# Performance work log

Hardware: AMD Instinct MI355X
Metric: run time of the kernel (lower is better)

The kernel has to match this reference:

```python
import jax, jax.numpy as jnp
import numpy as np

H = 256          # hidden_dim
D = 64           # dim_dynamic
R = 49           # pooler_resolution ** 2
N = 2000         # bs * num_proposals
EPS = 1e-5


def _ln(x, g, b):
    m = jnp.mean(x, axis=-1, keepdims=True)
    v = jnp.mean(jnp.square(x - m), axis=-1, keepdims=True)
    return (x - m) * jax.lax.rsqrt(v + EPS) * g + b


def setup_inputs() -> dict:
    key = jax.random.key(0)
    ks = jax.random.split(key, 6)
    pro_features = jax.random.normal(ks[0], (1, N, H), dtype=jnp.float32)
    roi_features = jax.random.normal(ks[1], (R, N, H), dtype=jnp.float32)
    # dynamic_layer: Linear(H, num_dynamic * H * D) with num_dynamic = 2
    W_dyn = jax.random.normal(ks[2], (H, 2 * H * D), dtype=jnp.float32) * 0.02
    b_dyn = jnp.zeros((2 * H * D,), dtype=jnp.float32)
    # out_layer: Linear(H * R, H)
    W_out = jax.random.normal(ks[3], (H * R, H), dtype=jnp.float32) * 0.02
    b_out = jnp.zeros((H,), dtype=jnp.float32)
    g1 = jnp.ones((D,), dtype=jnp.float32); b1 = jnp.zeros((D,), dtype=jnp.float32)
    g2 = jnp.ones((H,), dtype=jnp.float32); b2 = jnp.zeros((H,), dtype=jnp.float32)
    g3 = jnp.ones((H,), dtype=jnp.float32); b3 = jnp.zeros((H,), dtype=jnp.float32)
    return {"pro_features": pro_features, "roi_features": roi_features,
            "W_dyn": W_dyn, "b_dyn": b_dyn, "W_out": W_out, "b_out": b_out,
            "g1": g1, "b1": b1, "g2": g2, "b2": b2, "g3": g3, "b3": b3}


def reference(pro_features, roi_features, W_dyn, b_dyn, W_out, b_out,
              g1, b1, g2, b2, g3, b3):
    # roi_features: (R, N, H) -> features: (N, R, H)
    feats = jnp.transpose(roi_features, (1, 0, 2))
    # per-instance dynamic parameters: (N, 2*H*D)
    params = pro_features[0] @ W_dyn + b_dyn
    num_params = H * D
    p1 = params[:, :num_params].reshape(-1, H, D)   # (N, H, D)
    p2 = params[:, num_params:].reshape(-1, D, H)   # (N, D, H)
    f = jnp.einsum('nrh,nhd->nrd', feats, p1)       # bmm 1
    f = jax.nn.relu(_ln(f, g1, b1))
    f = jnp.einsum('nrd,ndh->nrh', f, p2)           # bmm 2
    f = jax.nn.relu(_ln(f, g2, b2))
    f = f.reshape(f.shape[0], R * H)                # flatten(1)
    f = jax.nn.relu(_ln(f @ W_out + b_out, g3, b3))
    return f  # (N, H)
```

## Files before the change

### kernel.cpp

```cpp
#include <hip/hip_runtime.h>

typedef unsigned short u16;
typedef __attribute__((ext_vector_type(8))) short short8;
typedef __attribute__((ext_vector_type(4))) float f32x4;

#define N_INST 2000
#define H_DIM 256
#define D_DIM 64
#define R_DIM 49
#define LN_EPS 1e-5f
#define SPLITK 14

__device__ __forceinline__ u16 f2bf(float f) {
  union { float f; unsigned int i; } x; x.f = f;
  unsigned int r = x.i + 0x7fffu + ((x.i >> 16) & 1u);
  return (u16)(r >> 16);
}
__device__ __forceinline__ float bf2f(u16 u) {
  union { unsigned int i; float f; } x; x.i = ((unsigned int)u) << 16; return x.f;
}
__device__ __forceinline__ short8 ld8(const u16* p) {
  return *reinterpret_cast<const short8*>(p);
}
__device__ __forceinline__ short8 pack8(float4 a, float4 b) {
  short8 r;
  r[0] = (short)f2bf(a.x); r[1] = (short)f2bf(a.y);
  r[2] = (short)f2bf(a.z); r[3] = (short)f2bf(a.w);
  r[4] = (short)f2bf(b.x); r[5] = (short)f2bf(b.y);
  r[6] = (short)f2bf(b.z); r[7] = (short)f2bf(b.w);
  return r;
}
__device__ __forceinline__ f32x4 mfma16(short8 a, short8 b, f32x4 c) {
  return __builtin_amdgcn_mfma_f32_16x16x32_bf16(a, b, c, 0, 0, 0);
}
__device__ __forceinline__ void gload16(const u16* g, u16* l) {
  __builtin_amdgcn_global_load_lds(
      (const __attribute__((address_space(1))) void*)g,
      (__attribute__((address_space(3))) void*)l, 16, 0, 0);
}

__global__ __launch_bounds__(256) void prep_all(
    const float* __restrict__ pro,  u16* __restrict__ proB,
    const float* __restrict__ Wdyn, u16* __restrict__ WdynT,
    const float* __restrict__ Wout, u16* __restrict__ WoutT) {
  __shared__ u16 T[64][65];
  const int tid = threadIdx.x;
  const int wave = tid >> 6, lane = tid & 63;
  const int b = blockIdx.x;
  if (b < 2048) {
    const int half = b >> 10;
    const int bb = b & 1023;
    const int kt = bb >> 8;
    long colbase, rowbase; int rstride;
    if (half == 0) {
      int h = bb & 255;
      colbase = (long)h * 64; rowbase = h; rstride = 256;
    } else {
      int d = bb & 63, hc = (bb >> 6) & 3;
      colbase = 16384L + d * 256 + hc * 64;
      rowbase = 16384L + hc * 4096 + d; rstride = 64;
    }
#pragma unroll
    for (int i = 0; i < 16; ++i) {
      int kk = wave * 16 + i;
      int k = kt * 64 + kk;
      T[kk][lane] = f2bf(Wdyn[(long)k * 32768 + colbase + lane]);
    }
    __syncthreads();
#pragma unroll
    for (int i = 0; i < 16; ++i) {
      int jj = wave * 16 + i;
      long ro = rowbase + (long)jj * rstride;
      WdynT[ro * 256 + kt * 64 + lane] = T[lane][jj];
    }
  } else if (b < 2832) {
    const int b2 = b - 2048;
    const int kt = b2 >> 2, ct = b2 & 3;
#pragma unroll
    for (int i = 0; i < 16; ++i) {
      int kk = wave * 16 + i;
      long k = (long)kt * 64 + kk;
      T[kk][lane] = f2bf(Wout[k * 256 + ct * 64 + lane]);
    }
    __syncthreads();
#pragma unroll
    for (int i = 0; i < 16; ++i) {
      int cc = wave * 16 + i;
      long c = (long)ct * 64 + cc;
      WoutT[c * 12544 + (long)kt * 64 + lane] = T[lane][cc];
    }
  } else {
    const int n4 = 128000;
    for (int i = (b - 2832) * 256 + tid; i < n4; i += 500 * 256) {
      float4 v = ((const float4*)pro)[i];
      u16* op = proB + i * 4;
      op[0] = f2bf(v.x); op[1] = f2bf(v.y); op[2] = f2bf(v.z); op[3] = f2bf(v.w);
    }
  }
}

__global__ __launch_bounds__(256, 3) void gemm128(
    const u16* __restrict__ A, int lda, int M,
    const u16* __restrict__ BT, int ldbt,
    const float* __restrict__ bias, int bias_mode,
    void* __restrict__ Cout, int ldc, long c_stride_s,
    int ksteps, int n_blocks, int out_f32)
{
  union Smem {
    struct { u16 a[2][128 * 32]; u16 b[2][128 * 32]; } s;
    u16 cb[128 * 128];
  };
  __shared__ Smem sm;

  const int tid = threadIdx.x;
  const int wave = tid >> 6, lane = tid & 63;
  const int quad = lane >> 4, l16 = lane & 15;
  const int wm = wave >> 1, wn = wave & 1;
  const int bid = blockIdx.x;
  const int mblk = bid / n_blocks, nblk = bid - mblk * n_blocks;
  const int m0 = mblk * 128, n0 = nblk * 128;
  const int s = blockIdx.y;
  const int kb = s * ksteps * 32;

  const int cl = tid & 3;
  const int r0 = tid >> 2, r1 = 64 + (tid >> 2);
  const int cg0 = cl ^ ((r0 >> 1) & 3);
  const int cg1 = cl ^ ((r1 >> 1) & 3);
  int ga0 = m0 + r0; if (ga0 >= M) ga0 = M - 1;
  int ga1 = m0 + r1; if (ga1 >= M) ga1 = M - 1;
  const u16* gA0 = A + (long)ga0 * lda + kb + cg0 * 8;
  const u16* gA1 = A + (long)ga1 * lda + kb + cg1 * 8;
  const u16* gB0 = BT + (long)(n0 + r0) * ldbt + kb + cg0 * 8;
  const u16* gB1 = BT + (long)(n0 + r1) * ldbt + kb + cg1 * 8;

  int fAoff[4], fBoff[4];
#pragma unroll
  for (int i = 0; i < 4; ++i) {
    int rt = wm * 64 + i * 16 + l16;
    fAoff[i] = rt * 32 + (quad ^ ((rt >> 1) & 3)) * 8;
    int ct = wn * 64 + i * 16 + l16;
    fBoff[i] = ct * 32 + (quad ^ ((ct >> 1) & 3)) * 8;
  }

  f32x4 acc[4][4];
#pragma unroll
  for (int mi = 0; mi < 4; ++mi)
#pragma unroll
    for (int ni = 0; ni < 4; ++ni) acc[mi][ni] = f32x4{0.f, 0.f, 0.f, 0.f};

  gload16(gA0, &sm.s.a[0][tid * 8]);
  gload16(gA1, &sm.s.a[0][(tid + 256) * 8]);
  gload16(gB0, &sm.s.b[0][tid * 8]);
  gload16(gB1, &sm.s.b[0][(tid + 256) * 8]);

  for (int ks = 0; ks < ksteps; ++ks) {
    const int cur = ks & 1, nxt = cur ^ 1;
    __syncthreads();
    if (ks + 1 < ksteps) {
      const int ko = (ks + 1) * 32;
      gload16(gA0 + ko, &sm.s.a[nxt][tid * 8]);
      gload16(gA1 + ko, &sm.s.a[nxt][(tid + 256) * 8]);
      gload16(gB0 + ko, &sm.s.b[nxt][tid * 8]);
      gload16(gB1 + ko, &sm.s.b[nxt][(tid + 256) * 8]);
    }
    short8 av[4], bv[4];
#pragma unroll
    for (int i = 0; i < 4; ++i) {
      av[i] = ld8(&sm.s.a[cur][fAoff[i]]);
      bv[i] = ld8(&sm.s.b[cur][fBoff[i]]);
    }
#pragma unroll
    for (int mi = 0; mi < 4; ++mi)
#pragma unroll
      for (int ni = 0; ni < 4; ++ni)
        acc[mi][ni] = mfma16(av[mi], bv[ni], acc[mi][ni]);
  }

  if (!out_f32) {
    float bvv[4];
#pragma unroll
    for (int ni = 0; ni < 4; ++ni) {
      int col = n0 + wn * 64 + ni * 16 + l16;
      int bi = col;
      if (bias_mode == 3)
        bi = (col < 16384) ? (((col & 255) << 6) + (col >> 8))
                           : (16384 + ((col & 63) << 8) + ((col >> 6) & 255));
      bvv[ni] = bias ? bias[bi] : 0.f;
    }
    __syncthreads();
#pragma unroll
    for (int mi = 0; mi < 4; ++mi)
#pragma unroll
      for (int ni = 0; ni < 4; ++ni)
#pragma unroll
        for (int i = 0; i < 4; ++i) {
          int row = wm * 64 + mi * 16 + quad * 4 + i;
          int col = wn * 64 + ni * 16 + l16;
          sm.cb[row * 128 + col] = f2bf(acc[mi][ni][i] + bvv[ni]);
        }
    __syncthreads();
    u16* Cp = (u16*)Cout;
#pragma unroll
    for (int j = 0; j < 8; ++j) {
      int lin = j * 2048 + tid * 8;
      int row = lin >> 7, col = lin & 127;
      int grow = m0 + row;
      if (grow < M)
        *reinterpret_cast<short8*>(Cp + (long)grow * ldc + n0 + col) =
            ld8(&sm.cb[lin]);
    }
  } else {
    float* Cp = (float*)Cout + (long)s * c_stride_s;
#pragma unroll
    for (int mi = 0; mi < 4; ++mi)
#pragma unroll
      for (int ni = 0; ni < 4; ++ni) {
        int col = n0 + wn * 64 + ni * 16 + l16;
#pragma unroll
        for (int i = 0; i < 4; ++i) {
          int row = m0 + wm * 64 + mi * 16 + quad * 4 + i;
          if (row < M) Cp[(long)row * ldc + col] = acc[mi][ni][i];
        }
      }
  }
}

__global__ __launch_bounds__(256, 4) void bmm12_ln(
    const float* __restrict__ roi,
    const u16* __restrict__ P12,
    const float* __restrict__ g1, const float* __restrict__ b1,
    const float* __restrict__ g2, const float* __restrict__ b2,
    u16* __restrict__ f2n)
{
  __shared__ __align__(16) u16 p1b[16384];
  __shared__ __align__(16) u16 f1b[4096];
  const int n = blockIdx.x;
  const int tid = threadIdx.x;
  const int wave = tid >> 6, lane = tid & 63;
  const int quad = lane >> 4, l16 = lane & 15;
  const int wstripe = wave * 16;

  const u16* P1n = P12 + (long)n * 32768;
#pragma unroll
  for (int j = 0; j < 8; ++j) {
    int lc = j * 256 + tid;
    int d = lc >> 5, c = lc & 31;
    int cg = (c & 24) | ((c & 7) ^ (d & 7));
    gload16(P1n + d * 256 + cg * 8, &p1b[lc * 8]);
  }
  int r = wstripe + l16;
  int rr = (r < R_DIM) ? r : 0;
  const float* Arow = roi + ((long)rr * N_INST + n) * H_DIM + quad * 8;
  short8 sa[8];
#pragma unroll
  for (int ks = 0; ks < 8; ++ks) {
    float4 va = ((const float4*)(Arow + ks * 32))[0];
    float4 vb = ((const float4*)(Arow + ks * 32))[1];
    sa[ks] = pack8(va, vb);
  }
  const u16* P2n = P12 + (long)n * 32768 + 16384;
  short8 pf[4][2];
#pragma unroll
  for (int hs = 0; hs < 4; ++hs)
#pragma unroll
    for (int ks = 0; ks < 2; ++ks) {
      int h = wave * 64 + hs * 16 + l16;
      pf[hs][ks] = ld8(P2n + h * 64 + (ks * 4 + quad) * 8);
    }
  float gv1[4], bv1[4];
#pragma unroll
  for (int sub = 0; sub < 4; ++sub) {
    gv1[sub] = g1[sub * 16 + l16]; bv1[sub] = b1[sub * 16 + l16];
  }
  __syncthreads();

  f32x4 acc1[4];
#pragma unroll
  for (int i = 0; i < 4; ++i) acc1[i] = f32x4{0.f, 0.f, 0.f, 0.f};
#pragma unroll
  for (int ks = 0; ks < 8; ++ks) {
#pragma unroll
    for (int sub = 0; sub < 4; ++sub) {
      int d = sub * 16 + l16;
      int q = ks * 4 + quad;
      int c = (q & 24) | ((q & 7) ^ (d & 7));
      acc1[sub] = mfma16(sa[ks], ld8(&p1b[d * 256 + c * 8]), acc1[sub]);
    }
  }

  {
    float s1[4], s2[4];
#pragma unroll
    for (int i = 0; i < 4; ++i) {
      s1[i] = 0.f; s2[i] = 0.f;
#pragma unroll
      for (int sub = 0; sub < 4; ++sub) {
        float v = acc1[sub][i]; s1[i] += v; s2[i] += v * v;
      }
    }
#pragma unroll
    for (int m = 1; m < 16; m <<= 1)
#pragma unroll
      for (int i = 0; i < 4; ++i) {
        s1[i] += __shfl_xor(s1[i], m, 16);
        s2[i] += __shfl_xor(s2[i], m, 16);
      }
#pragma unroll
    for (int i = 0; i < 4; ++i) {
      float mean = s1[i] * (1.f / 64.f);
      float var = s2[i] * (1.f / 64.f) - mean * mean;
      float rs = rsqrtf(var + LN_EPS);
      int row = wstripe + quad * 4 + i;
#pragma unroll
      for (int sub = 0; sub < 4; ++sub) {
        float y = fmaxf((acc1[sub][i] - mean) * rs * gv1[sub] + bv1[sub], 0.f);
        int kc = (sub * 2 + (l16 >> 3)) ^ (row & 7);
        f1b[row * 64 + kc * 8 + (l16 & 7)] = f2bf(y);
      }
    }
  }
  __syncthreads();

  f32x4 acc2[4][4];
#pragma unroll
  for (int rs = 0; rs < 4; ++rs)
#pragma unroll
    for (int hs = 0; hs < 4; ++hs) acc2[rs][hs] = f32x4{0.f, 0.f, 0.f, 0.f};
#pragma unroll
  for (int ks = 0; ks < 2; ++ks) {
#pragma unroll
    for (int rs = 0; rs < 4; ++rs) {
      int row = rs * 16 + l16;
      int c2 = (ks * 4 + quad) ^ (row & 7);
      short8 af = ld8(&f1b[row * 64 + c2 * 8]);
#pragma unroll
      for (int hs = 0; hs < 4; ++hs)
        acc2[rs][hs] = mfma16(af, pf[hs][ks], acc2[rs][hs]);
    }
  }

  float s1[4][4], s2[4][4];
#pragma unroll
  for (int rs = 0; rs < 4; ++rs)
#pragma unroll
    for (int i = 0; i < 4; ++i) {
      float a = 0.f, b = 0.f;
#pragma unroll
      for (int hs = 0; hs < 4; ++hs) {
        float v = acc2[rs][hs][i]; a += v; b += v * v;
      }
      s1[rs][i] = a; s2[rs][i] = b;
    }
#pragma unroll
  for (int m = 1; m < 16; m <<= 1)
#pragma unroll
    for (int rs = 0; rs < 4; ++rs)
#pragma unroll
      for (int i = 0; i < 4; ++i) {
        s1[rs][i] += __shfl_xor(s1[rs][i], m, 16);
        s2[rs][i] += __shfl_xor(s2[rs][i], m, 16);
      }
  float2* lnst = reinterpret_cast<float2*>(&p1b[14336]);
  if (l16 == 0) {
#pragma unroll
    for (int rs = 0; rs < 4; ++rs)
#pragma unroll
      for (int i = 0; i < 4; ++i) {
        int row = rs * 16 + quad * 4 + i;
        lnst[row * 4 + wave] = float2{s1[rs][i], s2[rs][i]};
      }
  }
  __syncthreads();

#pragma unroll
  for (int rs = 0; rs < 4; ++rs)
#pragma unroll
    for (int i = 0; i < 4; ++i) {
      int row = rs * 16 + quad * 4 + i;
      f32x4 qa = *reinterpret_cast<const f32x4*>(&lnst[row * 4]);
      f32x4 qb = *reinterpret_cast<const f32x4*>(&lnst[row * 4 + 2]);
      float S1 = qa[0] + qa[2] + qb[0] + qb[2];
      float S2 = qa[1] + qa[3] + qb[1] + qb[3];
      float mean = S1 * (1.f / 256.f);
      float var = S2 * (1.f / 256.f) - mean * mean;
      float rsq = rsqrtf(var + LN_EPS);
      if (row < R_DIM) {
#pragma unroll
        for (int hs = 0; hs < 4; ++hs)
          p1b[row * 264 + wave * 64 + hs * 16 + l16] =
              f2bf((acc2[rs][hs][i] - mean) * rsq);
      }
    }
  __syncthreads();

  u16* f2out = f2n + (long)n * (R_DIM * H_DIM);
  for (int t = tid; t < R_DIM * 32; t += 256) {
    int row = t >> 5, c = t & 31;
    short8 z8 = ld8(&p1b[row * 264 + c * 8]);
    const float4* gp = (const float4*)(g2 + c * 8);
    const float4* bp = (const float4*)(b2 + c * 8);
    float4 ga = gp[0], gb = gp[1], ba = bp[0], bb = bp[1];
    short8 y;
    y[0] = (short)f2bf(fmaxf(bf2f((u16)z8[0]) * ga.x + ba.x, 0.f));
    y[1] = (short)f2bf(fmaxf(bf2f((u16)z8[1]) * ga.y + ba.y, 0.f));
    y[2] = (short)f2bf(fmaxf(bf2f((u16)z8[2]) * ga.z + ba.z, 0.f));
    y[3] = (short)f2bf(fmaxf(bf2f((u16)z8[3]) * ga.w + ba.w, 0.f));
    y[4] = (short)f2bf(fmaxf(bf2f((u16)z8[4]) * gb.x + bb.x, 0.f));
    y[5] = (short)f2bf(fmaxf(bf2f((u16)z8[5]) * gb.y + bb.y, 0.f));
    y[6] = (short)f2bf(fmaxf(bf2f((u16)z8[6]) * gb.z + bb.z, 0.f));
    y[7] = (short)f2bf(fmaxf(bf2f((u16)z8[7]) * gb.w + bb.w, 0.f));
    *reinterpret_cast<short8*>(f2out + row * 256 + c * 8) = y;
  }
}

__global__ __launch_bounds__(256) void ln3_k(
    const float* __restrict__ partial,
    const float* __restrict__ b_out,
    const float* __restrict__ g3, const float* __restrict__ b3,
    float* __restrict__ out)
{
  const int n = blockIdx.x * 8 + (threadIdx.x >> 5);
  const int t = threadIdx.x & 31;
  const int h0 = t * 8;
  float4 xa = ((const float4*)(b_out + h0))[0];
  float4 xb = ((const float4*)(b_out + h0))[1];
#pragma unroll
  for (int ss = 0; ss < SPLITK; ++ss) {
    const float* pp = partial + ((long)ss * N_INST + n) * H_DIM + h0;
    float4 va = ((const float4*)pp)[0];
    float4 vb = ((const float4*)pp)[1];
    xa.x += va.x; xa.y += va.y; xa.z += va.z; xa.w += va.w;
    xb.x += vb.x; xb.y += vb.y; xb.z += vb.z; xb.w += vb.w;
  }
  float sv = xa.x + xa.y + xa.z + xa.w + xb.x + xb.y + xb.z + xb.w;
  float s2 = xa.x * xa.x + xa.y * xa.y + xa.z * xa.z + xa.w * xa.w +
             xb.x * xb.x + xb.y * xb.y + xb.z * xb.z + xb.w * xb.w;
#pragma unroll
  for (int m = 1; m < 32; m <<= 1) {
    sv += __shfl_xor(sv, m, 32);
    s2 += __shfl_xor(s2, m, 32);
  }
  float mean = sv * (1.f / 256.f);
  float var = s2 * (1.f / 256.f) - mean * mean;
  float rs = rsqrtf(var + LN_EPS);
  float4 ga = ((const float4*)(g3 + h0))[0];
  float4 gb = ((const float4*)(g3 + h0))[1];
  float4 ba = ((const float4*)(b3 + h0))[0];
  float4 bb = ((const float4*)(b3 + h0))[1];
  float4 ya, yb;
  ya.x = fmaxf((xa.x - mean) * rs * ga.x + ba.x, 0.f);
  ya.y = fmaxf((xa.y - mean) * rs * ga.y + ba.y, 0.f);
  ya.z = fmaxf((xa.z - mean) * rs * ga.z + ba.z, 0.f);
  ya.w = fmaxf((xa.w - mean) * rs * ga.w + ba.w, 0.f);
  yb.x = fmaxf((xb.x - mean) * rs * gb.x + bb.x, 0.f);
  yb.y = fmaxf((xb.y - mean) * rs * gb.y + bb.y, 0.f);
  yb.z = fmaxf((xb.z - mean) * rs * gb.z + bb.z, 0.f);
  yb.w = fmaxf((xb.w - mean) * rs * gb.w + bb.w, 0.f);
  float* op = out + (long)n * H_DIM + h0;
  ((float4*)op)[0] = ya;
  ((float4*)op)[1] = yb;
}

extern "C" void kernel_launch(void* const* d_in, const int* in_sizes, int n_in,
                              void* d_out, int out_size, void* d_ws, size_t ws_size,
                              hipStream_t stream) {
  const float* pro  = (const float*)d_in[0];
  const float* roi  = (const float*)d_in[1];
  const float* Wdyn = (const float*)d_in[2];
  const float* bdyn = (const float*)d_in[3];
  const float* Wout = (const float*)d_in[4];
  const float* bout = (const float*)d_in[5];
  const float* g1 = (const float*)d_in[6];
  const float* b1 = (const float*)d_in[7];
  const float* g2 = (const float*)d_in[8];
  const float* b2 = (const float*)d_in[9];
  const float* g3 = (const float*)d_in[10];
  const float* b3 = (const float*)d_in[11];
  float* out = (float*)d_out;

  char* ws = (char*)d_ws;
  u16* proB  = (u16*)ws;
  u16* WdynT = (u16*)(ws + 1024000);
  u16* WoutT = (u16*)(ws + 17801216);
  u16* P12   = (u16*)(ws + 24223744);
  u16* f2n   = (u16*)(ws + 155295744);
  float* partial = (float*)(ws + 24223744);

  dim3 blk(256);

  prep_all<<<dim3(3332), blk, 0, stream>>>(pro, proB, Wdyn, WdynT, Wout, WoutT);

  gemm128<<<dim3(16 * 256, 1), blk, 0, stream>>>(
      proB, H_DIM, N_INST, WdynT, H_DIM, bdyn, 3,
      (void*)P12, 32768, 0L, 8, 256, 0);

  bmm12_ln<<<dim3(N_INST), blk, 0, stream>>>(roi, P12, g1, b1, g2, b2, f2n);

  gemm128<<<dim3(16 * 2, SPLITK), blk, 0, stream>>>(
      f2n, R_DIM * H_DIM, N_INST, WoutT, R_DIM * H_DIM, nullptr, 0,
      (void*)partial, H_DIM, (long)N_INST * H_DIM, 28, 2, 1);

  ln3_k<<<dim3(250), blk, 0, stream>>>(partial, bout, g3, b3, out);
}
```

Before: 322.7 us.

## Process two instances per block and prefetch the second's operands during the first

The per-instance bmm/LayerNorm kernel now handles two proposals per block, using double-buffered LDS for P1 and F1. It issues the async global-to-LDS P1 loads, the ROI feature loads and the P2 loads for the second instance before computing the first, so memory latency overlaps with compute. Some __syncthreads are replaced by manual waitcnt plus s_barrier. In exchange LDS use doubles, register pressure rises (occupancy hint drops from 4 to 2 blocks) and there are half as many blocks.

```diff
diff --git a/kernel.cpp b/kernel.cpp
--- a/kernel.cpp
+++ b/kernel.cpp
@@ -225,191 +225,375 @@
   }
 }
 
-__global__ __launch_bounds__(256, 4) void bmm12_ln(
+__global__ __launch_bounds__(256, 2) void bmm12_ln2(
     const float* __restrict__ roi,
     const u16* __restrict__ P12,
     const float* __restrict__ g1, const float* __restrict__ b1,
     const float* __restrict__ g2, const float* __restrict__ b2,
     u16* __restrict__ f2n)
 {
-  __shared__ __align__(16) u16 p1b[16384];
-  __shared__ __align__(16) u16 f1b[4096];
-  const int n = blockIdx.x;
+  __shared__ __align__(16) u16 p1b[2][16384];
+  __shared__ __align__(16) u16 f1b[2][4096];
   const int tid = threadIdx.x;
   const int wave = tid >> 6, lane = tid & 63;
   const int quad = lane >> 4, l16 = lane & 15;
   const int wstripe = wave * 16;
-
-  const u16* P1n = P12 + (long)n * 32768;
+  const int n0 = blockIdx.x * 2;
+
+  float gv1[4], bv1[4];
+#pragma unroll
+  for (int sub = 0; sub < 4; ++sub) {
+    gv1[sub] = g1[sub * 16 + l16]; bv1[sub] = b1[sub * 16 + l16];
+  }
+  int r = wstripe + l16;
+  int rr = (r < R_DIM) ? r : 0;
+  const float* Arow0 = roi + ((long)rr * N_INST + n0) * H_DIM + quad * 8;
+  float4 rv0[16];
+#pragma unroll
+  for (int ks = 0; ks < 8; ++ks) {
+    rv0[2 * ks]     = ((const float4*)(Arow0 + ks * 32))[0];
+    rv0[2 * ks + 1] = ((const float4*)(Arow0 + ks * 32))[1];
+  }
+  const u16* P2n0 = P12 + (long)n0 * 32768 + 16384;
+  short8 pf0[4][2];
+#pragma unroll
+  for (int hs = 0; hs < 4; ++hs)
+#pragma unroll
+    for (int ks = 0; ks < 2; ++ks) {
+      int h = wave * 64 + hs * 16 + l16;
+      pf0[hs][ks] = ld8(P2n0 + h * 64 + (ks * 4 + quad) * 8);
+    }
+  const u16* P1n0 = P12 + (long)n0 * 32768;
 #pragma unroll
   for (int j = 0; j < 8; ++j) {
     int lc = j * 256 + tid;
     int d = lc >> 5, c = lc & 31;
     int cg = (c & 24) | ((c & 7) ^ (d & 7));
-    gload16(P1n + d * 256 + cg * 8, &p1b[lc * 8]);
-  }
-  int r = wstripe + l16;
-  int rr = (r < R_DIM) ? r : 0;
-  const float* Arow = roi + ((long)rr * N_INST + n) * H_DIM + quad * 8;
-  short8 sa[8];
+    gload16(P1n0 + d * 256 + cg * 8, &p1b[0][lc * 8]);
+  }
+  __builtin_amdgcn_sched_barrier(0);
+  const u16* P1n1 = P12 + (long)(n0 + 1) * 32768;
+#pragma unroll
+  for (int j = 0; j < 8; ++j) {
+    int lc = j * 256 + tid;
+    int d = lc >> 5, c = lc & 31;
+    int cg = (c & 24) | ((c & 7) ^ (d & 7));
+    gload16(P1n1 + d * 256 + cg * 8, &p1b[1][lc * 8]);
+  }
+  __builtin_amdgcn_sched_barrier(0);
+  asm volatile("s_waitcnt vmcnt(8)" ::: "memory");
+  __builtin_amdgcn_s_barrier();
+
+  short8 sa0[8];
+#pragma unroll
+  for (int ks = 0; ks < 8; ++ks) sa0[ks] = pack8(rv0[2 * ks], rv0[2 * ks + 1]);
+
+  const float* Arow1 = roi + ((long)rr * N_INST + (n0 + 1)) * H_DIM + quad * 8;
+  float4 rv1[16];
 #pragma unroll
   for (int ks = 0; ks < 8; ++ks) {
-    float4 va = ((const float4*)(Arow + ks * 32))[0];
-    float4 vb = ((const float4*)(Arow + ks * 32))[1];
-    sa[ks] = pack8(va, vb);
-  }
-  const u16* P2n = P12 + (long)n * 32768 + 16384;
-  short8 pf[4][2];
+    rv1[2 * ks]     = ((const float4*)(Arow1 + ks * 32))[0];
+    rv1[2 * ks + 1] = ((const float4*)(Arow1 + ks * 32))[1];
+  }
+  const u16* P2n1 = P12 + (long)(n0 + 1) * 32768 + 16384;
+  short8 pf1[4][2];
 #pragma unroll
   for (int hs = 0; hs < 4; ++hs)
 #pragma unroll
     for (int ks = 0; ks < 2; ++ks) {
       int h = wave * 64 + hs * 16 + l16;
-      pf[hs][ks] = ld8(P2n + h * 64 + (ks * 4 + quad) * 8);
-    }
-  float gv1[4], bv1[4];
-#pragma unroll
-  for (int sub = 0; sub < 4; ++sub) {
-    gv1[sub] = g1[sub * 16 + l16]; bv1[sub] = b1[sub * 16 + l16];
-  }
+      pf1[hs][ks] = ld8(P2n1 + h * 64 + (ks * 4 + quad) * 8);
+    }
+
+  short8 sa1[8];
+
+  {
+    u16* p1 = p1b[0];
+    u16* f1 = f1b[0];
+    f32x4 acc1[4];
+#pragma unroll
+    for (int i = 0; i < 4; ++i) acc1[i] = f32x4{0.f, 0.f, 0.f, 0.f};
+#pragma unroll
+    for (int ks = 0; ks < 8; ++ks) {
+#pragma unroll
+      for (int sub = 0; sub < 4; ++sub) {
+        int d = sub * 16 + l16;
+        int q = ks * 4 + quad;
+        int c = (q & 24) | ((q & 7) ^ (d & 7));
+        acc1[sub] = mfma16(sa0[ks], ld8(&p1[d * 256 + c * 8]), acc1[sub]);
+      }
+    }
+    {
+      float s1[4], s2[4];
+#pragma unroll
+      for (int i = 0; i < 4; ++i) {
+        s1[i] = 0.f; s2[i] = 0.f;
+#pragma unroll
+        for (int sub = 0; sub < 4; ++sub) {
+          float v = acc1[sub][i]; s1[i] += v; s2[i] += v * v;
+        }
+      }
+#pragma unroll
+      for (int m = 1; m < 16; m <<= 1)
+#pragma unroll
+        for (int i = 0; i < 4; ++i) {
+          s1[i] += __shfl_xor(s1[i], m, 16);
+          s2[i] += __shfl_xor(s2[i], m, 16);
+        }
+#pragma unroll
+      for (int i = 0; i < 4; ++i) {
+        float mean = s1[i] * (1.f / 64.f);
+        float var = s2[i] * (1.f / 64.f) - mean * mean;
+        float rs = rsqrtf(var + LN_EPS);
+        int row = wstripe + quad * 4 + i;
+#pragma unroll
+        for (int sub = 0; sub < 4; ++sub) {
+          float y = fmaxf((acc1[sub][i] - mean) * rs * gv1[sub] + bv1[sub], 0.f);
+          int kc = (sub * 2 + (l16 >> 3)) ^ (row & 7);
+          f1[row * 64 + kc * 8 + (l16 & 7)] = f2bf(y);
+        }
+      }
+    }
+    asm volatile("s_waitcnt lgkmcnt(0)" ::: "memory");
+    __builtin_amdgcn_s_barrier();
+
+#pragma unroll
+    for (int ks = 0; ks < 8; ++ks)
+      sa1[ks] = pack8(rv1[2 * ks], rv1[2 * ks + 1]);
+
+    f32x4 acc2[4][4];
+#pragma unroll
+    for (int rs = 0; rs < 4; ++rs)
+#pragma unroll
+      for (int hs = 0; hs < 4; ++hs) acc2[rs][hs] = f32x4{0.f, 0.f, 0.f, 0.f};
+#pragma unroll
+    for (int ks = 0; ks < 2; ++ks) {
+#pragma unroll
+      for (int rs = 0; rs < 4; ++rs) {
+        int row = rs * 16 + l16;
+        int c2 = (ks * 4 + quad) ^ (row & 7);
+        short8 af = ld8(&f1[row * 64 + c2 * 8]);
+#pragma unroll
+        for (int hs = 0; hs < 4; ++hs)
+          acc2[rs][hs] = mfma16(af, pf0[hs][ks], acc2[rs][hs]);
+      }
+    }
+    float s1[4][4], s2[4][4];
+#pragma unroll
+    for (int rs = 0; rs < 4; ++rs)
+#pragma unroll
+      for (int i = 0; i < 4; ++i) {
+        float a = 0.f, b = 0.f;
+#pragma unroll
+        for (int hs = 0; hs < 4; ++hs) {
+          float v = acc2[rs][hs][i]; a += v; b += v * v;
+        }
+        s1[rs][i] = a; s2[rs][i] = b;
+      }
+#pragma unroll
+    for (int m = 1; m < 16; m <<= 1)
+#pragma unroll
+      for (int rs = 0; rs < 4; ++rs)
+#pragma unroll
+        for (int i = 0; i < 4; ++i) {
+          s1[rs][i] += __shfl_xor(s1[rs][i], m, 16);
+          s2[rs][i] += __shfl_xor(s2[rs][i], m, 16);
+        }
+    float2* lnst = reinterpret_cast<float2*>(&p1[14336]);
+    if (l16 == 0) {
+#pragma unroll
+      for (int rs = 0; rs < 4; ++rs)
+#pragma unroll
+        for (int i = 0; i < 4; ++i) {
+          int row = rs * 16 + quad * 4 + i;
+          lnst[row * 4 + wave] = float2{s1[rs][i], s2[rs][i]};
+        }
+    }
+    asm volatile("s_waitcnt lgkmcnt(0)" ::: "memory");
+    __builtin_amdgcn_s_barrier();
+
+#pragma unroll
+    for (int rs = 0; rs < 4; ++rs)
+#pragma unroll
+      for (int i = 0; i < 4; ++i) {
+        int row = rs * 16 + quad * 4 + i;
+        f32x4 qa = *reinterpret_cast<const f32x4*>(&lnst[row * 4]);
+        f32x4 qb = *reinterpret_cast<const f32x4*>(&lnst[row * 4 + 2]);
+        float S1 = qa[0] + qa[2] + qb[0] + qb[2];
+        float S2 = qa[1] + qa[3] + qb[1] + qb[3];
+        float mean = S1 * (1.f / 256.f);
+        float var = S2 * (1.f / 256.f) - mean * mean;
+        float rsq = rsqrtf(var + LN_EPS);
+        if (row < R_DIM) {
+#pragma unroll
+          for (int hs = 0; hs < 4; ++hs)
+            p1[row * 264 + wave * 64 + hs * 16 + l16] =
+                f2bf((acc2[rs][hs][i] - mean) * rsq);
+        }
+      }
+    asm volatile("s_waitcnt lgkmcnt(0)" ::: "memory");
+    __builtin_amdgcn_s_barrier();
+
+    u16* f2out = f2n + (long)n0 * (R_DIM * H_DIM);
+    for (int t = tid; t < R_DIM * 32; t += 256) {
+      int row = t >> 5, c = t & 31;
+      short8 z8 = ld8(&p1[row * 264 + c * 8]);
+      const float4* gp = (const float4*)(g2 + c * 8);
+      const float4* bp = (const float4*)(b2 + c * 8);
+      float4 ga = gp[0], gb = gp[1], ba = bp[0], bb = bp[1];
+      short8 y;
+      y[0] = (short)f2bf(fmaxf(bf2f((u16)z8[0]) * ga.x + ba.x, 0.f));
+      y[1] = (short)f2bf(fmaxf(bf2f((u16)z8[1]) * ga.y + ba.y, 0.f));
+      y[2] = (short)f2bf(fmaxf(bf2f((u16)z8[2]) * ga.z + ba.z, 0.f));
+      y[3] = (short)f2bf(fmaxf(bf2f((u16)z8[3]) * ga.w + ba.w, 0.f));
+      y[4] = (short)f2bf(fmaxf(bf2f((u16)z8[4]) * gb.x + bb.x, 0.f));
+      y[5] = (short)f2bf(fmaxf(bf2f((u16)z8[5]) * gb.y + bb.y, 0.f));
+      y[6] = (short)f2bf(fmaxf(bf2f((u16)z8[6]) * gb.z + bb.z, 0.f));
+      y[7] = (short)f2bf(fmaxf(bf2f((u16)z8[7]) * gb.w + bb.w, 0.f));
+      *reinterpret_cast<short8*>(f2out + row * 256 + c * 8) = y;
+    }
+  }
+
   __syncthreads();
 
-  f32x4 acc1[4];
-#pragma unroll
-  for (int i = 0; i < 4; ++i) acc1[i] = f32x4{0.f, 0.f, 0.f, 0.f};
-#pragma unroll
-  for (int ks = 0; ks < 8; ++ks) {
-#pragma unroll
-    for (int sub = 0; sub < 4; ++sub) {
-      int d = sub * 16 + l16;
-      int q = ks * 4 + quad;
-      int c = (q & 24) | ((q & 7) ^ (d & 7));
-      acc1[sub] = mfma16(sa[ks], ld8(&p1b[d * 256 + c * 8]), acc1[sub]);
-    }
-  }
-
   {
-    float s1[4], s2[4];
-#pragma unroll
-    for (int i = 0; i < 4; ++i) {
-      s1[i] = 0.f; s2[i] = 0.f;
+    u16* p1 = p1b[1];
+    u16* f1 = f1b[1];
+    f32x4 acc1[4];
+#pragma unroll
+    for (int i = 0; i < 4; ++i) acc1[i] = f32x4{0.f, 0.f, 0.f, 0.f};
+#pragma unroll
+    for (int ks = 0; ks < 8; ++ks) {
 #pragma unroll
       for (int sub = 0; sub < 4; ++sub) {
-        float v = acc1[sub][i]; s1[i] += v; s2[i] += v * v;
-      }
-    }
+        int d = sub * 16 + l16;
+        int q = ks * 4 + quad;
+        int c = (q & 24) | ((q & 7) ^ (d & 7));
+        acc1[sub] = mfma16(sa1[ks], ld8(&p1[d * 256 + c * 8]), acc1[sub]);
+      }
+    }
+    {
+      float s1[4], s2[4];
+#pragma unroll
+      for (int i = 0; i < 4; ++i) {
+        s1[i] = 0.f; s2[i] = 0.f;
+#pragma unroll
+        for (int sub = 0; sub < 4; ++sub) {
+          float v = acc1[sub][i]; s1[i] += v; s2[i] += v * v;
+        }
+      }
+#pragma unroll
+      for (int m = 1; m < 16; m <<= 1)
+#pragma unroll
+        for (int i = 0; i < 4; ++i) {
+          s1[i] += __shfl_xor(s1[i], m, 16);
+          s2[i] += __shfl_xor(s2[i], m, 16);
+        }
+#pragma unroll
+      for (int i = 0; i < 4; ++i) {
+        float mean = s1[i] * (1.f / 64.f);
+        float var = s2[i] * (1.f / 64.f) - mean * mean;
+        float rs = rsqrtf(var + LN_EPS);
+        int row = wstripe + quad * 4 + i;
+#pragma unroll
+        for (int sub = 0; sub < 4; ++sub) {
+          float y = fmaxf((acc1[sub][i] - mean) * rs * gv1[sub] + bv1[sub], 0.f);
+          int kc = (sub * 2 + (l16 >> 3)) ^ (row & 7);
+          f1[row * 64 + kc * 8 + (l16 & 7)] = f2bf(y);
+        }
+      }
+    }
+    __syncthreads();
+
+    f32x4 acc2[4][4];
+#pragma unroll
+    for (int rs = 0; rs < 4; ++rs)
+#pragma unroll
+      for (int hs = 0; hs < 4; ++hs) acc2[rs][hs] = f32x4{0.f, 0.f, 0.f, 0.f};
+#pragma unroll
+    for (int ks = 0; ks < 2; ++ks) {
+#pragma unroll
+      for (int rs = 0; rs < 4; ++rs) {
+        int row = rs * 16 + l16;
+        int c2 = (ks * 4 + quad) ^ (row & 7);
+        short8 af = ld8(&f1[row * 64 + c2 * 8]);
+#pragma unroll
+        for (int hs = 0; hs < 4; ++hs)
+          acc2[rs][hs] = mfma16(af, pf1[hs][ks], acc2[rs][hs]);
+      }
+    }
+    float s1[4][4], s2[4][4];
+#pragma unroll
+    for (int rs = 0; rs < 4; ++rs)
+#pragma unroll
+      for (int i = 0; i < 4; ++i) {
+        float a = 0.f, b = 0.f;
+#pragma unroll
+        for (int hs = 0; hs < 4; ++hs) {
+          float v = acc2[rs][hs][i]; a += v; b += v * v;
+        }
+        s1[rs][i] = a; s2[rs][i] = b;
+      }
 #pragma unroll
     for (int m = 1; m < 16; m <<= 1)
 #pragma unroll
-      for (int i = 0; i < 4; ++i) {
-        s1[i] += __shfl_xor(s1[i], m, 16);
-        s2[i] += __shfl_xor(s2[i], m, 16);
-      }
-#pragma unroll
-    for (int i = 0; i < 4; ++i) {
-      float mean = s1[i] * (1.f / 64.f);
-      float var = s2[i] * (1.f / 64.f) - mean * mean;
-      float rs = rsqrtf(var + LN_EPS);
-      int row = wstripe + quad * 4 + i;
-#pragma unroll
-      for (int sub = 0; sub < 4; ++sub) {
-        float y = fmaxf((acc1[sub][i] - mean) * rs * gv1[sub] + bv1[sub], 0.f);
-        int kc = (sub * 2 + (l16 >> 3)) ^ (row & 7);
-        f1b[row * 64 + kc * 8 + (l16 & 7)] = f2bf(y);
-      }
-    }
-  }
-  __syncthreads();
-
-  f32x4 acc2[4][4];
-#pragma unroll
-  for (int rs = 0; rs < 4; ++rs)
-#pragma unroll
-    for (int hs = 0; hs < 4; ++hs) acc2[rs][hs] = f32x4{0.f, 0.f, 0.f, 0.f};
-#pragma unroll
-  for (int ks = 0; ks < 2; ++ks) {
-#pragma unroll
-    for (int rs = 0; rs < 4; ++rs) {
-      int row = rs * 16 + l16;
-      int c2 = (ks * 4 + quad) ^ (row & 7);
-      short8 af = ld8(&f1b[row * 64 + c2 * 8]);
-#pragma unroll
-      for (int hs = 0; hs < 4; ++hs)
-        acc2[rs][hs] = mfma16(af, pf[hs][ks], acc2[rs][hs]);
-    }
-  }
-
-  float s1[4][4], s2[4][4];
-#pragma unroll
-  for (int rs = 0; rs < 4; ++rs)
-#pragma unroll
-    for (int i = 0; i < 4; ++i) {
-      float a = 0.f, b = 0.f;
-#pragma unroll
-      for (int hs = 0; hs < 4; ++hs) {
-        float v = acc2[rs][hs][i]; a += v; b += v * v;
-      }
-      s1[rs][i] = a; s2[rs][i] = b;
-    }
-#pragma unroll
-  for (int m = 1; m < 16; m <<= 1)
+      for (int rs = 0; rs < 4; ++rs)
+#pragma unroll
+        for (int i = 0; i < 4; ++i) {
+          s1[rs][i] += __shfl_xor(s1[rs][i], m, 16);
+          s2[rs][i] += __shfl_xor(s2[rs][i], m, 16);
+        }
+    float2* lnst = reinterpret_cast<float2*>(&p1[14336]);
+    if (l16 == 0) {
+#pragma unroll
+      for (int rs = 0; rs < 4; ++rs)
+#pragma unroll
+        for (int i = 0; i < 4; ++i) {
+          int row = rs * 16 + quad * 4 + i;
+          lnst[row * 4 + wave] = float2{s1[rs][i], s2[rs][i]};
+        }
+    }
+    __syncthreads();
+
 #pragma unroll
     for (int rs = 0; rs < 4; ++rs)
 #pragma unroll
       for (int i = 0; i < 4; ++i) {
-        s1[rs][i] += __shfl_xor(s1[rs][i], m, 16);
-        s2[rs][i] += __shfl_xor(s2[rs][i], m, 16);
-      }
-  float2* lnst = reinterpret_cast<float2*>(&p1b[14336]);
-  if (l16 == 0) {
-#pragma unroll
-    for (int rs = 0; rs < 4; ++rs)
-#pragma unroll
-      for (int i = 0; i < 4; ++i) {
         int row = rs * 16 + quad * 4 + i;
-        lnst[row * 4 + wave] = float2{s1[rs][i], s2[rs][i]};
-      }
-  }
-  __syncthreads();
-
-#pragma unroll
-  for (int rs = 0; rs < 4; ++rs)
-#pragma unroll
-    for (int i = 0; i < 4; ++i) {
-      int row = rs * 16 + quad * 4 + i;
-      f32x4 qa = *reinterpret_cast<const f32x4*>(&lnst[row * 4]);
-      f32x4 qb = *reinterpret_cast<const f32x4*>(&lnst[row * 4 + 2]);
-      float S1 = qa[0] + qa[2] + qb[0] + qb[2];
-      float S2 = qa[1] + qa[3] + qb[1] + qb[3];
-      float mean = S1 * (1.f / 256.f);
-      float var = S2 * (1.f / 256.f) - mean * mean;
-      float rsq = rsqrtf(var + LN_EPS);
-      if (row < R_DIM) {
-#pragma unroll
-        for (int hs = 0; hs < 4; ++hs)
-          p1b[row * 264 + wave * 64 + hs * 16 + l16] =
-              f2bf((acc2[rs][hs][i] - mean) * rsq);
-      }
-    }
-  __syncthreads();
-
-  u16* f2out = f2n + (long)n * (R_DIM * H_DIM);
-  for (int t = tid; t < R_DIM * 32; t += 256) {
-    int row = t >> 5, c = t & 31;
-    short8 z8 = ld8(&p1b[row * 264 + c * 8]);
-    const float4* gp = (const float4*)(g2 + c * 8);
-    const float4* bp = (const float4*)(b2 + c * 8);
-    float4 ga = gp[0], gb = gp[1], ba = bp[0], bb = bp[1];
-    short8 y;
-    y[0] = (short)f2bf(fmaxf(bf2f((u16)z8[0]) * ga.x + ba.x, 0.f));
-    y[1] = (short)f2bf(fmaxf(bf2f((u16)z8[1]) * ga.y + ba.y, 0.f));
-    y[2] = (short)f2bf(fmaxf(bf2f((u16)z8[2]) * ga.z + ba.z, 0.f));
-    y[3] = (short)f2bf(fmaxf(bf2f((u16)z8[3]) * ga.w + ba.w, 0.f));
-    y[4] = (short)f2bf(fmaxf(bf2f((u16)z8[4]) * gb.x + bb.x, 0.f));
-    y[5] = (short)f2bf(fmaxf(bf2f((u16)z8[5]) * gb.y + bb.y, 0.f));
-    y[6] = (short)f2bf(fmaxf(bf2f((u16)z8[6]) * gb.z + bb.z, 0.f));
-    y[7] = (short)f2bf(fmaxf(bf2f((u16)z8[7]) * gb.w + bb.w, 0.f));
-    *reinterpret_cast<short8*>(f2out + row * 256 + c * 8) = y;
+        f32x4 qa = *reinterpret_cast<const f32x4*>(&lnst[row * 4]);
+        f32x4 qb = *reinterpret_cast<const f32x4*>(&lnst[row * 4 + 2]);
+        float S1 = qa[0] + qa[2] + qb[0] + qb[2];
+        float S2 = qa[1] + qa[3] + qb[1] + qb[3];
+        float mean = S1 * (1.f / 256.f);
+        float var = S2 * (1.f / 256.f) - mean * mean;
+        float rsq = rsqrtf(var + LN_EPS);
+        if (row < R_DIM) {
+#pragma unroll
+          for (int hs = 0; hs < 4; ++hs)
+            p1[row * 264 + wave * 64 + hs * 16 + l16] =
+                f2bf((acc2[rs][hs][i] - mean) * rsq);
+        }
+      }
+    __syncthreads();
+
+    u16* f2out = f2n + (long)(n0 + 1) * (R_DIM * H_DIM);
+    for (int t = tid; t < R_DIM * 32; t += 256) {
+      int row = t >> 5, c = t & 31;
+      short8 z8 = ld8(&p1[row * 264 + c * 8]);
+      const float4* gp = (const float4*)(g2 + c * 8);
+      const float4* bp = (const float4*)(b2 + c * 8);
+      float4 ga = gp[0], gb = gp[1], ba = bp[0], bb = bp[1];
+      short8 y;
+      y[0] = (short)f2bf(fmaxf(bf2f((u16)z8[0]) * ga.x + ba.x, 0.f));
+      y[1] = (short)f2bf(fmaxf(bf2f((u16)z8[1]) * ga.y + ba.y, 0.f));
+      y[2] = (short)f2bf(fmaxf(bf2f((u16)z8[2]) * ga.z + ba.z, 0.f));
+      y[3] = (short)f2bf(fmaxf(bf2f((u16)z8[3]) * ga.w + ba.w, 0.f));
+      y[4] = (short)f2bf(fmaxf(bf2f((u16)z8[4]) * gb.x + bb.x, 0.f));
+      y[5] = (short)f2bf(fmaxf(bf2f((u16)z8[5]) * gb.y + bb.y, 0.f));
+      y[6] = (short)f2bf(fmaxf(bf2f((u16)z8[6]) * gb.z + bb.z, 0.f));
+      y[7] = (short)f2bf(fmaxf(bf2f((u16)z8[7]) * gb.w + bb.w, 0.f));
+      *reinterpret_cast<short8*>(f2out + row * 256 + c * 8) = y;
+    }
   }
 }
 
@@ -494,7 +678,7 @@
       proB, H_DIM, N_INST, WdynT, H_DIM, bdyn, 3,
       (void*)P12, 32768, 0L, 8, 256, 0);
 
-  bmm12_ln<<<dim3(N_INST), blk, 0, stream>>>(roi, P12, g1, b1, g2, b2, f2n);
+  bmm12_ln2<<<dim3(N_INST / 2), blk, 0, stream>>>(roi, P12, g1, b1, g2, b2, f2n);
 
   gemm128<<<dim3(16 * 2, SPLITK), blk, 0, stream>>>(
       f2n, R_DIM * H_DIM, N_INST, WoutT, R_DIM * H_DIM, nullptr, 0,
```

Measured after the change: 334.3 us. 1.04x slower.
